# Kernel optimization log

Hardware: AMD Instinct MI355X
Metric: run time of the kernel (lower is better)

Reference implementation:

```python
import jax, jax.numpy as jnp
import numpy as np
from jax import lax

DN = ('NCHW', 'OIHW', 'NCHW')

def _winit(key, fan_in, shape):
    return (jax.random.uniform(key, shape) - 0.5) * 2 * 2.4 / fan_in ** 0.5

def setup_inputs() -> dict:
    key = jax.random.key(0)
    ks = jax.random.split(key, 6)
    B = 131072
    x = jax.random.normal(ks[0], (B, 1, 16, 16), dtype=jnp.float32)
    H1w = _winit(ks[1], 5 * 5 * 1, (12, 1, 5, 5))
    H1b = jnp.zeros((12, 8, 8), jnp.float32)
    H2w = _winit(ks[2], 5 * 5 * 8, (12, 8, 5, 5))
    H2b = jnp.zeros((12, 4, 4), jnp.float32)
    H3w = _winit(ks[3], 4 * 4 * 12, (4 * 4 * 12, 30))
    H3b = jnp.zeros((30,), jnp.float32)
    outw = _winit(ks[4], 30, (30, 10))
    outb = jnp.zeros((10,), jnp.float32)
    return {"x": x, "H1w": H1w, "H1b": H1b, "H2w": H2w, "H2b": H2b,
            "H3w": H3w, "H3b": H3b, "outw": outw, "outb": outb}

def _pad_m1(x):
    # constant pad of 2 on H and W with value -1.0
    return jnp.pad(x, ((0, 0), (0, 0), (2, 2), (2, 2)), constant_values=-1.0)

def _conv_s2(x, w):
    return lax.conv_general_dilated(x, w, window_strides=(2, 2),
                                    padding='VALID', dimension_numbers=DN)

def reference(x, H1w, H1b, H2w, H2b, H3w, H3b, outw, outb):
    # eval mode: no roll augmentation, dropout is identity
    x = _pad_m1(x)                                   # [B,1,20,20]
    x = _conv_s2(x, H1w) + H1b                       # [B,12,8,8]
    x = jax.nn.relu(x)
    x = _pad_m1(x)                                   # [B,12,12,12]
    s1 = _conv_s2(x[:, 0:8], H2w[0:4])               # [B,4,4,4]
    s2 = _conv_s2(x[:, 4:12], H2w[4:8])              # [B,4,4,4]
    s3 = _conv_s2(jnp.concatenate((x[:, 0:4], x[:, 8:12]), axis=1), H2w[8:12])
    x = jnp.concatenate((s1, s2, s3), axis=1) + H2b  # [B,12,4,4]
    x = jax.nn.relu(x)
    x = x.reshape(x.shape[0], -1)                    # [B,192]
    x = jax.nn.relu(x @ H3w + H3b)                   # [B,30]
    return x @ outw + outb                           # [B,10]
```

## Files before the change

kernel.cpp:

```cpp
#include <hip/hip_runtime.h>
#include <hip/hip_fp16.h>

typedef _Float16 f16x8 __attribute__((ext_vector_type(8)));
typedef float f32x4 __attribute__((ext_vector_type(4)));

union U4H8 { uint4 u; f16x8 h; };
__device__ inline f16x8 asH(uint4 u){ U4H8 x; x.u = u; return x.h; }
__device__ inline unsigned int pk(float a, float b){
    __half2 h = __floats2half2_rn(a, b);
    union { __half2 h; unsigned int u; } c; c.h = h; return c.u;
}
__device__ inline unsigned short h16(float a){
    union { __half h; unsigned short s; } c; c.h = __float2half(a); return c.s;
}

#define NFRAG 28
#define WS_B1 7168
#define WS_B2 8192

__global__ __launch_bounds__(256) void build_tables(
    const float* __restrict__ H1w, const float* __restrict__ H1b,
    const float* __restrict__ H2w, const float* __restrict__ H2b,
    const float* __restrict__ H3w, const float* __restrict__ outw,
    unsigned int* __restrict__ ws)
{
    const int t = threadIdx.x, b = blockIdx.x;
    float* wsf = (float*)ws;

    if (b < NFRAG) {
        if (t < 64) {
            const int lane = t, ch = lane >> 4, oc = lane & 15;
            const int fi = b;
            unsigned short us[8];
            for (int j = 0; j < 8; ++j) {
                float w = 0.f;
                if (fi < 2) {
                    int kh = fi * 4 + ch;
                    if (kh < 5 && j < 5 && oc < 12) w = H1w[oc * 25 + kh * 5 + j];
                } else if (fi < 15) {
                    int kk = fi - 2;
                    int tap = kk * 2 + (ch >> 1);
                    int ic = (ch & 1) * 8 + j;
                    if (tap < 25 && oc < 12) {
                        int kh = tap / 5, kw = tap % 5;
                        int q = oc >> 2, icl = -1;
                        if (q == 0)      { if (ic < 8) icl = ic; }
                        else if (q == 1) { if (ic >= 4 && ic < 12) icl = ic - 4; }
                        else             { if (ic < 4) icl = ic;
                                           else if (ic >= 8 && ic < 12) icl = ic - 4; }
                        if (icl >= 0) w = H2w[((oc * 8 + icl) * 5 + kh) * 5 + kw];
                    }
                } else if (fi < 27) {
                    int idx = fi - 15, nt = idx / 6, kk = idx % 6;
                    int k = kk * 32 + ch * 8 + j;
                    int pos = k / 12, oc2 = k % 12;
                    int col = nt * 16 + oc;
                    if (col < 30) w = H3w[(oc2 * 16 + pos) * 30 + col];
                } else {
                    int k = ch * 8 + j;
                    if (k < 30 && oc < 10) w = outw[k * 10 + oc];
                }
                us[j] = h16(w);
            }
            uint4 u;
            u.x = us[0] | ((unsigned int)us[1] << 16);
            u.y = us[2] | ((unsigned int)us[3] << 16);
            u.z = us[4] | ((unsigned int)us[5] << 16);
            u.w = us[6] | ((unsigned int)us[7] << 16);
            ((uint4*)ws)[fi * 64 + lane] = u;
        }
    } else if (b == NFRAG) {
        for (int idx = t; idx < 1024; idx += 256) {
            int e = idx >> 6, l2 = idx & 63;
            int tt = e >> 2, r = e & 3;
            int oc = 4 * (l2 >> 4) + r, m2 = l2 & 15;
            int oh = 2 * tt + (m2 >> 3), ow = m2 & 7;
            float v = 0.f;
            if (oc < 12) {
                v = H1b[oc * 64 + oh * 8 + ow];
                for (int kh = 0; kh < 5; ++kh)
                    for (int kw = 0; kw < 5; ++kw) {
                        int rr = 2 * oh + kh, cc = 2 * ow + kw;
                        if (rr < 2 || rr >= 18 || cc < 2 || cc >= 18)
                            v -= H1w[oc * 25 + kh * 5 + kw];
                    }
            }
            wsf[WS_B1 + e * 64 + l2] = v;
        }
    } else {
        int e = t >> 6, l2 = t & 63;
        int oc = 4 * (l2 >> 4) + e, m2 = l2 & 15;
        int oh = m2 >> 2, ow = m2 & 3;
        float v = 0.f;
        if (oc < 12) {
            v = H2b[oc * 16 + oh * 4 + ow];
            for (int icl = 0; icl < 8; ++icl)
                for (int kh = 0; kh < 5; ++kh)
                    for (int kw = 0; kw < 5; ++kw) {
                        int rr = 2 * oh + kh - 2, cc = 2 * ow + kw - 2;
                        if (rr < 0 || rr >= 8 || cc < 0 || cc >= 8)
                            v -= H2w[((oc * 8 + icl) * 5 + kh) * 5 + kw];
                    }
        }
        wsf[WS_B2 + e * 64 + l2] = v;
    }
}

#define SLICE 10112
__global__ __launch_bounds__(256, 4) void modernnet_mfma(
    const float* __restrict__ x, const unsigned int* __restrict__ ws,
    const float* __restrict__ H3b, const float* __restrict__ outb,
    float* __restrict__ out)
{
    __shared__ uint4 lds4[4 * SLICE / 16];
    const int t = threadIdx.x, wave = t >> 6, l = t & 63;
    const int ch = l >> 4, m = l & 15;
    char* base = (char*)lds4 + wave * SLICE;
    const int s0 = blockIdx.x * 8 + wave * 2;

    const uint4* fr = (const uint4*)ws;
    const float* wsf = (const float*)ws;

    uint4 c1b0 = fr[0 * 64 + l], c1b1 = fr[1 * 64 + l];
    f32x4 b1f[4];
    #pragma unroll
    for (int tt = 0; tt < 4; ++tt)
        #pragma unroll
        for (int r = 0; r < 4; ++r) b1f[tt][r] = wsf[WS_B1 + (tt * 4 + r) * 64 + l];

    int c2off[13];
    {
        const int mb = 24 * (m >> 2) + 2 * (m & 3);
        const int hb = (ch & 1) << 4;
        #pragma unroll
        for (int kk = 0; kk < 13; ++kk) {
            int tap = kk * 2 + (ch >> 1); if (tap > 24) tap = 24;
            int kh = tap / 5, kw = tap % 5;
            int pos = mb + kh * 12 + kw;
            c2off[kk] = ((pos << 5) + hb) ^ ((pos & 12) << 2);
        }
    }

    {
        uint4 z; z.x = z.y = z.z = z.w = 0u;
        ((uint4*)base)[l] = z;
        if (l < 56) ((uint4*)base)[64 + l] = z;
    }

    {
        const float* xp = x + (size_t)s0 * 256 + l * 8;
        float4 v0 = *(const float4*)xp;
        float4 v1 = *(const float4*)(xp + 4);
        int sI = l >> 5, idx = l & 31;
        int r = idx >> 1, c = (idx & 1) * 8;
        char* dst = base + sI * 960 + (r + 2) * 48 + (c + 2) * 2;
        ((unsigned int*)dst)[0] = pk(v0.x, v0.y);
        ((unsigned int*)dst)[1] = pk(v0.z, v0.w);
        ((unsigned int*)dst)[2] = pk(v1.x, v1.y);
        ((unsigned int*)dst)[3] = pk(v1.z, v1.w);
    }

    f32x4 acc1[8];
    #pragma unroll
    for (int i = 0; i < 8; ++i) {
        const int s = i >> 2, tt = i & 3;
        const char* ap = base + s * 960 + (2 * tt + (m >> 3)) * 96 + (m & 7) * 4;
        const unsigned int* p0 = (const unsigned int*)(ap + ch * 48);
        uint4 b0 = make_uint4(p0[0], p0[1], p0[2], p0[3]);
        uint4 b1 = make_uint4(0u, 0u, 0u, 0u);
        if (ch == 0) {
            const unsigned int* p1 = (const unsigned int*)(ap + 192);
            b1 = make_uint4(p1[0], p1[1], p1[2], p1[3]);
        }
        f32x4 acc = b1f[tt];
        acc = __builtin_amdgcn_mfma_f32_16x16x32_f16(asH(c1b0), asH(b0), acc, 0, 0, 0);
        acc = __builtin_amdgcn_mfma_f32_16x16x32_f16(asH(c1b1), asH(b1), acc, 0, 0, 0);
        acc1[i] = acc;
    }

    #pragma unroll
    for (int i = 0; i < 8; ++i) {
        const int s = i >> 2, tt = i & 3;
        const int pos = (2 * tt + (m >> 3) + 2) * 12 + (m & 7) + 2;
        const int off = ((pos << 5) + ch * 8) ^ ((pos & 12) << 2);
        unsigned int w0 = pk(fmaxf(acc1[i][0], 0.f), fmaxf(acc1[i][1], 0.f));
        unsigned int w1 = pk(fmaxf(acc1[i][2], 0.f), fmaxf(acc1[i][3], 0.f));
        *(uint2*)(base + s * 4608 + off) = make_uint2(w0, w1);
    }

    uint4 c2b[13];
    #pragma unroll
    for (int kk = 0; kk < 13; ++kk) c2b[kk] = fr[(2 + kk) * 64 + l];
    f32x4 b2f;
    #pragma unroll
    for (int r = 0; r < 4; ++r) b2f[r] = wsf[WS_B2 + r * 64 + l];

    {
        uint4 z; z.x = z.y = z.z = z.w = 0u;
        #pragma unroll
        for (int k2 = 0; k2 < 5; ++k2) {
            int idx = l + k2 * 64;
            int smp = (idx >= 160) ? 1 : 0;
            int ci = idx - smp * 160;
            int pi = ci >> 1, half = ci & 1;
            int pos;
            if (pi < 24) pos = pi;
            else if (pi < 48) pos = pi + 96;
            else {
                int q = pi - 48;
                int c = q & 3; c = (c < 2) ? c : c + 8;
                pos = (2 + (q >> 2)) * 12 + c;
            }
            int off = ((pos << 5) + (half << 4)) ^ ((pos & 12) << 2);
            *(uint4*)(base + smp * 4608 + off) = z;
        }
    }

    #pragma unroll
    for (int s = 0; s < 2; ++s) {
        const char* hb1 = base + s * 4608;
        f32x4 acc = b2f;
        #pragma unroll
        for (int kk = 0; kk < 13; ++kk) {
            uint4 a = *(const uint4*)(hb1 + c2off[kk]);
            acc = __builtin_amdgcn_mfma_f32_16x16x32_f16(asH(c2b[kk]), asH(a), acc, 0, 0, 0);
        }
        if (ch < 3) {
            unsigned int w0 = pk(fmaxf(acc[0], 0.f), fmaxf(acc[1], 0.f));
            unsigned int w1 = pk(fmaxf(acc[2], 0.f), fmaxf(acc[3], 0.f));
            *(uint2*)(base + 9216 + s * 384 + m * 24 + ch * 8) = make_uint2(w0, w1);
        }
    }

    #pragma unroll
    for (int nt = 0; nt < 2; ++nt) {
        const int jb = nt * 16 + 4 * ch;
        f32x4 acc;
        #pragma unroll
        for (int r = 0; r < 4; ++r) acc[r] = (jb + r < 30) ? H3b[jb + r] : 0.f;
        #pragma unroll
        for (int kk = 0; kk < 6; ++kk) {
            uint4 bw = fr[(15 + nt * 6 + kk) * 64 + l];
            uint4 aa = *(const uint4*)(base + 9216 + (m & 1) * 384 + kk * 64 + ch * 16);
            acc = __builtin_amdgcn_mfma_f32_16x16x32_f16(asH(bw), asH(aa), acc, 0, 0, 0);
        }
        if (m < 2) {
            unsigned int w0 = pk(fmaxf(acc[0], 0.f), fmaxf(acc[1], 0.f));
            unsigned int w1 = pk(fmaxf(acc[2], 0.f), fmaxf(acc[3], 0.f));
            *(uint2*)(base + 9984 + m * 64 + nt * 32 + ch * 8) = make_uint2(w0, w1);
        }
    }

    {
        uint4 bw = fr[27 * 64 + l];
        uint4 aa = *(const uint4*)(base + 9984 + (m & 1) * 64 + ch * 16);
        f32x4 acc;
        #pragma unroll
        for (int r = 0; r < 4; ++r) acc[r] = (4 * ch + r < 10) ? outb[4 * ch + r] : 0.f;
        acc = __builtin_amdgcn_mfma_f32_16x16x32_f16(asH(bw), asH(aa), acc, 0, 0, 0);
        if (m < 2) {
            float* op = out + (size_t)(s0 + m) * 10 + 4 * ch;
            if (ch < 2) {
                *(float2*)op       = make_float2(acc[0], acc[1]);
                *(float2*)(op + 2) = make_float2(acc[2], acc[3]);
            } else if (ch == 2) {
                *(float2*)op       = make_float2(acc[0], acc[1]);
            }
        }
    }
}

extern "C" void kernel_launch(void* const* d_in, const int* in_sizes, int n_in,
                              void* d_out, int out_size, void* d_ws, size_t ws_size,
                              hipStream_t stream) {
    const float* x    = (const float*)d_in[0];
    const float* H1w  = (const float*)d_in[1];
    const float* H1b  = (const float*)d_in[2];
    const float* H2w  = (const float*)d_in[3];
    const float* H2b  = (const float*)d_in[4];
    const float* H3w  = (const float*)d_in[5];
    const float* H3b  = (const float*)d_in[6];
    const float* outw = (const float*)d_in[7];
    const float* outb = (const float*)d_in[8];
    float* outp = (float*)d_out;
    unsigned int* ws = (unsigned int*)d_ws;

    build_tables<<<30, 256, 0, stream>>>(H1w, H1b, H2w, H2b, H3w, outw, ws);

    const int B = in_sizes[0] / 256;
    const int blocks = B / 8;
    modernnet_mfma<<<blocks, 256, 0, stream>>>(x, ws, H3b, outb, outp);
}
```

Measured before the change: 111.0 us.

## Share FC layers across block waves and interleave conv2 samples

The FC layers (H3 and the output layer) were computed separately by each wave for only 2 samples, which wasted most MFMA columns. They now run at block level: conv2 outputs for all 8 samples go to shared LDS, two waves compute the H3 tiles, and one wave computes the output layer, with __syncthreads barriers between stages. The H3 and output biases are pre-laid out into the workspace table, and the two conv2 samples are interleaved to expose MFMA ILP. The extra block barriers and idle waves in the tail stages may offset part of the gain.

```diff
diff --git a/kernel.cpp b/kernel.cpp
--- a/kernel.cpp
+++ b/kernel.cpp
@@ -17,11 +17,14 @@
 #define NFRAG 28
 #define WS_B1 7168
 #define WS_B2 8192
+#define WS_B3 8448
+#define WS_B4 8960
 
 __global__ __launch_bounds__(256) void build_tables(
     const float* __restrict__ H1w, const float* __restrict__ H1b,
     const float* __restrict__ H2w, const float* __restrict__ H2b,
-    const float* __restrict__ H3w, const float* __restrict__ outw,
+    const float* __restrict__ H3w, const float* __restrict__ H3b,
+    const float* __restrict__ outw, const float* __restrict__ outb,
     unsigned int* __restrict__ ws)
 {
     const int t = threadIdx.x, b = blockIdx.x;
@@ -88,35 +91,50 @@
             wsf[WS_B1 + e * 64 + l2] = v;
         }
     } else {
-        int e = t >> 6, l2 = t & 63;
-        int oc = 4 * (l2 >> 4) + e, m2 = l2 & 15;
-        int oh = m2 >> 2, ow = m2 & 3;
-        float v = 0.f;
-        if (oc < 12) {
-            v = H2b[oc * 16 + oh * 4 + ow];
-            for (int icl = 0; icl < 8; ++icl)
-                for (int kh = 0; kh < 5; ++kh)
-                    for (int kw = 0; kw < 5; ++kw) {
-                        int rr = 2 * oh + kh - 2, cc = 2 * ow + kw - 2;
-                        if (rr < 0 || rr >= 8 || cc < 0 || cc >= 8)
-                            v -= H2w[((oc * 8 + icl) * 5 + kh) * 5 + kw];
-                    }
-        }
-        wsf[WS_B2 + e * 64 + l2] = v;
-    }
-}
-
-#define SLICE 10112
+        {
+            int e = t >> 6, l2 = t & 63;
+            int oc = 4 * (l2 >> 4) + e, m2 = l2 & 15;
+            int oh = m2 >> 2, ow = m2 & 3;
+            float v = 0.f;
+            if (oc < 12) {
+                v = H2b[oc * 16 + oh * 4 + ow];
+                for (int icl = 0; icl < 8; ++icl)
+                    for (int kh = 0; kh < 5; ++kh)
+                        for (int kw = 0; kw < 5; ++kw) {
+                            int rr = 2 * oh + kh - 2, cc = 2 * ow + kw - 2;
+                            if (rr < 0 || rr >= 8 || cc < 0 || cc >= 8)
+                                v -= H2w[((oc * 8 + icl) * 5 + kh) * 5 + kw];
+                        }
+            }
+            wsf[WS_B2 + e * 64 + l2] = v;
+        }
+        for (int i = t; i < 512; i += 256) {
+            int e = i >> 6, l2 = i & 63;
+            int nt = e >> 2, r = e & 3, ch = l2 >> 4;
+            int j = nt * 16 + 4 * ch + r;
+            wsf[WS_B3 + e * 64 + l2] = (j < 30) ? H3b[j] : 0.f;
+        }
+        {
+            int e = t >> 6, l2 = t & 63, ch = l2 >> 4;
+            int j = 4 * ch + e;
+            wsf[WS_B4 + e * 64 + l2] = (j < 10) ? outb[j] : 0.f;
+        }
+    }
+}
+
+#define H2B 36864
+#define H3B 40064
 __global__ __launch_bounds__(256, 4) void modernnet_mfma(
     const float* __restrict__ x, const unsigned int* __restrict__ ws,
-    const float* __restrict__ H3b, const float* __restrict__ outb,
     float* __restrict__ out)
 {
-    __shared__ uint4 lds4[4 * SLICE / 16];
+    __shared__ uint4 lds4[2536];
+    char* L = (char*)lds4;
     const int t = threadIdx.x, wave = t >> 6, l = t & 63;
     const int ch = l >> 4, m = l & 15;
-    char* base = (char*)lds4 + wave * SLICE;
-    const int s0 = blockIdx.x * 8 + wave * 2;
+    char* base = L + wave * 9216;
+    const int sblk = blockIdx.x * 8;
+    const int s0 = sblk + wave * 2;
 
     const uint4* fr = (const uint4*)ws;
     const float* wsf = (const float*)ws;
@@ -132,11 +150,14 @@
     {
         const int mb = 24 * (m >> 2) + 2 * (m & 3);
         const int hb = (ch & 1) << 4;
+        const int sel = (ch >> 1) & 1;
         #pragma unroll
         for (int kk = 0; kk < 13; ++kk) {
-            int tap = kk * 2 + (ch >> 1); if (tap > 24) tap = 24;
-            int kh = tap / 5, kw = tap % 5;
-            int pos = mb + kh * 12 + kw;
+            const int t0 = 2 * kk;
+            const int t1 = (2 * kk + 1 <= 24) ? 2 * kk + 1 : 24;
+            const int p0 = (t0 / 5) * 12 + (t0 % 5);
+            const int p1 = (t1 / 5) * 12 + (t1 % 5);
+            int pos = mb + (sel ? p1 : p0);
             c2off[kk] = ((pos << 5) + hb) ^ ((pos & 12) << 2);
         }
     }
@@ -167,11 +188,8 @@
         const char* ap = base + s * 960 + (2 * tt + (m >> 3)) * 96 + (m & 7) * 4;
         const unsigned int* p0 = (const unsigned int*)(ap + ch * 48);
         uint4 b0 = make_uint4(p0[0], p0[1], p0[2], p0[3]);
-        uint4 b1 = make_uint4(0u, 0u, 0u, 0u);
-        if (ch == 0) {
-            const unsigned int* p1 = (const unsigned int*)(ap + 192);
-            b1 = make_uint4(p1[0], p1[1], p1[2], p1[3]);
-        }
+        const unsigned int* p1 = (const unsigned int*)(ap + 192);
+        uint4 b1 = make_uint4(p1[0], p1[1], p1[2], p1[3]);
         f32x4 acc = b1f[tt];
         acc = __builtin_amdgcn_mfma_f32_16x16x32_f16(asH(c1b0), asH(b0), acc, 0, 0, 0);
         acc = __builtin_amdgcn_mfma_f32_16x16x32_f16(asH(c1b1), asH(b1), acc, 0, 0, 0);
@@ -216,50 +234,63 @@
         }
     }
 
-    #pragma unroll
-    for (int s = 0; s < 2; ++s) {
-        const char* hb1 = base + s * 4608;
-        f32x4 acc = b2f;
+    {
+        const char* h0 = base;
+        const char* h1 = base + 4608;
+        f32x4 a0 = b2f, a1 = b2f;
         #pragma unroll
         for (int kk = 0; kk < 13; ++kk) {
-            uint4 a = *(const uint4*)(hb1 + c2off[kk]);
-            acc = __builtin_amdgcn_mfma_f32_16x16x32_f16(asH(c2b[kk]), asH(a), acc, 0, 0, 0);
+            uint4 r0 = *(const uint4*)(h0 + c2off[kk]);
+            uint4 r1 = *(const uint4*)(h1 + c2off[kk]);
+            a0 = __builtin_amdgcn_mfma_f32_16x16x32_f16(asH(c2b[kk]), asH(r0), a0, 0, 0, 0);
+            a1 = __builtin_amdgcn_mfma_f32_16x16x32_f16(asH(c2b[kk]), asH(r1), a1, 0, 0, 0);
         }
         if (ch < 3) {
+            unsigned int w0 = pk(fmaxf(a0[0], 0.f), fmaxf(a0[1], 0.f));
+            unsigned int w1 = pk(fmaxf(a0[2], 0.f), fmaxf(a0[3], 0.f));
+            *(uint2*)(L + H2B + (wave * 2 + 0) * 400 + m * 24 + ch * 8) = make_uint2(w0, w1);
+            w0 = pk(fmaxf(a1[0], 0.f), fmaxf(a1[1], 0.f));
+            w1 = pk(fmaxf(a1[2], 0.f), fmaxf(a1[3], 0.f));
+            *(uint2*)(L + H2B + (wave * 2 + 1) * 400 + m * 24 + ch * 8) = make_uint2(w0, w1);
+        }
+    }
+
+    uint4 afc[6];
+    if (wave < 2) {
+        #pragma unroll
+        for (int kk = 0; kk < 6; ++kk) afc[kk] = fr[(15 + wave * 6 + kk) * 64 + l];
+    }
+
+    __syncthreads();
+
+    if (wave < 2) {
+        const int nt = wave;
+        f32x4 acc;
+        #pragma unroll
+        for (int r = 0; r < 4; ++r) acc[r] = wsf[WS_B3 + (nt * 4 + r) * 64 + l];
+        #pragma unroll
+        for (int kk = 0; kk < 6; ++kk) {
+            uint4 bb = *(const uint4*)(L + H2B + (m & 7) * 400 + kk * 64 + ch * 16);
+            acc = __builtin_amdgcn_mfma_f32_16x16x32_f16(asH(afc[kk]), asH(bb), acc, 0, 0, 0);
+        }
+        if (m < 8) {
             unsigned int w0 = pk(fmaxf(acc[0], 0.f), fmaxf(acc[1], 0.f));
             unsigned int w1 = pk(fmaxf(acc[2], 0.f), fmaxf(acc[3], 0.f));
-            *(uint2*)(base + 9216 + s * 384 + m * 24 + ch * 8) = make_uint2(w0, w1);
-        }
-    }
-
-    #pragma unroll
-    for (int nt = 0; nt < 2; ++nt) {
-        const int jb = nt * 16 + 4 * ch;
+            *(uint2*)(L + H3B + m * 64 + nt * 32 + ch * 8) = make_uint2(w0, w1);
+        }
+    }
+
+    __syncthreads();
+
+    if (wave == 0) {
+        uint4 aw = fr[27 * 64 + l];
+        uint4 bb = *(const uint4*)(L + H3B + (m & 7) * 64 + ch * 16);
         f32x4 acc;
         #pragma unroll
-        for (int r = 0; r < 4; ++r) acc[r] = (jb + r < 30) ? H3b[jb + r] : 0.f;
-        #pragma unroll
-        for (int kk = 0; kk < 6; ++kk) {
-            uint4 bw = fr[(15 + nt * 6 + kk) * 64 + l];
-            uint4 aa = *(const uint4*)(base + 9216 + (m & 1) * 384 + kk * 64 + ch * 16);
-            acc = __builtin_amdgcn_mfma_f32_16x16x32_f16(asH(bw), asH(aa), acc, 0, 0, 0);
-        }
-        if (m < 2) {
-            unsigned int w0 = pk(fmaxf(acc[0], 0.f), fmaxf(acc[1], 0.f));
-            unsigned int w1 = pk(fmaxf(acc[2], 0.f), fmaxf(acc[3], 0.f));
-            *(uint2*)(base + 9984 + m * 64 + nt * 32 + ch * 8) = make_uint2(w0, w1);
-        }
-    }
-
-    {
-        uint4 bw = fr[27 * 64 + l];
-        uint4 aa = *(const uint4*)(base + 9984 + (m & 1) * 64 + ch * 16);
-        f32x4 acc;
-        #pragma unroll
-        for (int r = 0; r < 4; ++r) acc[r] = (4 * ch + r < 10) ? outb[4 * ch + r] : 0.f;
-        acc = __builtin_amdgcn_mfma_f32_16x16x32_f16(asH(bw), asH(aa), acc, 0, 0, 0);
-        if (m < 2) {
-            float* op = out + (size_t)(s0 + m) * 10 + 4 * ch;
+        for (int r = 0; r < 4; ++r) acc[r] = wsf[WS_B4 + r * 64 + l];
+        acc = __builtin_amdgcn_mfma_f32_16x16x32_f16(asH(aw), asH(bb), acc, 0, 0, 0);
+        if (m < 8) {
+            float* op = out + (size_t)(sblk + m) * 10 + 4 * ch;
             if (ch < 2) {
                 *(float2*)op       = make_float2(acc[0], acc[1]);
                 *(float2*)(op + 2) = make_float2(acc[2], acc[3]);
@@ -285,9 +316,9 @@
     float* outp = (float*)d_out;
     unsigned int* ws = (unsigned int*)d_ws;
 
-    build_tables<<<30, 256, 0, stream>>>(H1w, H1b, H2w, H2b, H3w, outw, ws);
+    build_tables<<<30, 256, 0, stream>>>(H1w, H1b, H2w, H2b, H3w, H3b, outw, outb, ws);
 
     const int B = in_sizes[0] / 256;
     const int blocks = B / 8;
-    modernnet_mfma<<<blocks, 256, 0, stream>>>(x, ws, H3b, outb, outp);
-}
+    modernnet_mfma<<<blocks, 256, 0, stream>>>(x, ws, outp);
+}
```

New measurement: 92.64 us. -16.6%, faster.
